# Kernel tuning notes

Hardware: AMD Instinct MI355X
Metric: run time of the kernel (lower is better)

Reference implementation:

```python
import jax, jax.numpy as jnp
import numpy as np

# --- static mask-construction config (mirrors FlexAttnFunc.init_mask args) ---
B = 1
L_F, L_H, L_W = 8, 20, 36      # latent_shape[2:]
A_F, A_H, A_W = 8, 1, 1        # action_shape[2:]
PATCH = (1, 2, 2)
CHUNK = 1
PAD = 176
WINDOW = 6
DIM, HEADS, DHEAD = 1536, 12, 128
EPS = 1e-5


def _make_ids():
    lf, lh, lw = L_F // PATCH[0], L_H // PATCH[1], L_W // PATCH[2]
    lat_seq = np.repeat(np.arange(B), lf * lh * lw)
    act_seq = np.repeat(np.arange(B), A_F * A_H * A_W)
    seq = np.concatenate([lat_seq, lat_seq, act_seq, act_seq])
    lat_fr = np.broadcast_to(np.arange(L_F)[None, :, None, None], (B, L_F, lh, lw)).reshape(-1)
    act_fr = np.broadcast_to(np.arange(A_F)[None, :, None, None], (B, A_F, A_H, A_W)).reshape(-1)
    fr = np.concatenate([lat_fr // CHUNK * 2] * 2 + [act_fr // CHUNK * 2 + 1] * 2)
    nz = np.concatenate([np.zeros_like(lat_fr), np.ones_like(lat_fr),
                         np.zeros_like(act_fr), np.ones_like(act_fr)])
    pad = np.full(PAD, -1, dtype=np.int64)
    return (np.concatenate([seq, pad]).astype(np.int32),
            np.concatenate([fr, pad]).astype(np.int32),
            np.concatenate([nz, pad]).astype(np.int32))


def setup_inputs() -> dict:
    key = jax.random.key(0)
    ks = jax.random.split(key, 8)
    seq, fr, nz = _make_ids()
    S = seq.shape[0]  # 3072
    sd = 0.02
    return {
        'x': jax.random.normal(ks[0], (1, S, DIM), jnp.float32),
        'Wq': jax.random.normal(ks[1], (DIM, DIM), jnp.float32) * sd,
        'bq': jnp.zeros((DIM,), jnp.float32),
        'Wk': jax.random.normal(ks[2], (DIM, DIM), jnp.float32) * sd,
        'bk': jnp.zeros((DIM,), jnp.float32),
        'Wv': jax.random.normal(ks[3], (DIM, DIM), jnp.float32) * sd,
        'bv': jnp.zeros((DIM,), jnp.float32),
        'gq': 1.0 + jax.random.normal(ks[4], (DIM,), jnp.float32) * sd,
        'gk': 1.0 + jax.random.normal(ks[5], (DIM,), jnp.float32) * sd,
        'Wo': jax.random.normal(ks[6], (DIM, DIM), jnp.float32) * sd,
        'bo': jnp.zeros((DIM,), jnp.float32),
        'seq_ids': jnp.asarray(seq),
        'frame_ids': jnp.asarray(fr),
        'noise_ids': jnp.asarray(nz),
        'window_size': WINDOW,
    }


def _rms(u, g):
    # torch.nn.RMSNorm over last dim (size heads*dim_head), elementwise affine
    return u * jax.lax.rsqrt(jnp.mean(u * u, axis=-1, keepdims=True) + EPS) * g


def _mask(seq_ids, frame_ids, noise_ids, window_size):
    sq, sk = seq_ids[:, None], seq_ids[None, :]
    fq, fk = frame_ids[:, None], frame_ids[None, :]
    nq, nk = noise_ids[:, None], noise_ids[None, :]
    seq_ok = (sq == sk) & (sq >= 0) & (sk >= 0)
    c2c = (nq == 1) & (nk == 1) & (fk <= fq)      # clean->clean, block causal incl self
    n2c = (nq == 0) & (nk == 1) & (fk < fq)       # noise->clean, causal excl self
    n2n = (nq == 0) & (nk == 0) & (fk == fq)      # noise->noise, same frame only
    win = jnp.abs(fq - fk) <= window_size
    return (c2c | n2c | n2n) & seq_ok & win


def reference(x, Wq, bq, Wk, bk, Wv, bv, gq, gk, Wo, bo,
              seq_ids, frame_ids, noise_ids, window_size):
    S = x.shape[1]
    q = _rms(x @ Wq + bq, gq)[0].reshape(S, HEADS, DHEAD)
    k = _rms(x @ Wk + bk, gk)[0].reshape(S, HEADS, DHEAD)
    v = (x @ Wv + bv)[0].reshape(S, HEADS, DHEAD)
    mask = _mask(seq_ids, frame_ids, noise_ids, window_size)  # [S,S] bool
    scores = jnp.einsum('qhd,khd->hqk', q, k) * (DHEAD ** -0.5)
    scores = jnp.where(mask[None], scores, jnp.float32(-1e9))
    attn = jax.nn.softmax(scores, axis=-1)
    o = jnp.einsum('hqk,khd->qhd', attn, v)
    # zero out padded (fully-masked) query rows
    o = o * (seq_ids >= 0).astype(o.dtype)[:, None, None]
    y = o.reshape(1, S, HEADS * DHEAD) @ Wo + bo
    return y
```

## Files before the change

kernel.cpp:

```cpp
#include <hip/hip_runtime.h>
#include <hip/hip_bf16.h>
#include <stdint.h>

typedef __bf16 bf16x8 __attribute__((ext_vector_type(8)));
typedef float f32x4 __attribute__((ext_vector_type(4)));

__device__ __forceinline__ unsigned short f2bf(float f) {
  union { float f; unsigned int u; } v; v.f = f;
  unsigned int u = v.u;
  unsigned int r = (u + 0x7fffu + ((u >> 16) & 1u)) >> 16;
  return (unsigned short)r;
}
__device__ __forceinline__ float bf2f(unsigned short s) {
  union { unsigned int u; float f; } v; v.u = ((unsigned int)s) << 16; return v.f;
}

__global__ __launch_bounds__(256) void setup(
    const float* __restrict__ x,
    const float* __restrict__ Wq, const float* __restrict__ Wk,
    const float* __restrict__ Wv, const float* __restrict__ Wo,
    const int* __restrict__ seq, const int* __restrict__ fr,
    const int* __restrict__ nz, const int* __restrict__ wsz,
    unsigned short* __restrict__ x_bf, unsigned short* __restrict__ wt,
    unsigned long long* __restrict__ tbm, unsigned char* __restrict__ mb,
    float* __restrict__ ssq, int S) {
  __shared__ __align__(16) unsigned char smu[16384];
  int b = blockIdx.x, tid = threadIdx.x;
  if (b < 1152) {
    int base = b * 1024 + tid;
    for (int j = 0; j < 4; j++) {
      int i = base + j * 256;
      float4 v = ((const float4*)x)[i];
      ushort4 o;
      o.x = f2bf(v.x); o.y = f2bf(v.y); o.z = f2bf(v.z); o.w = f2bf(v.w);
      ((ushort4*)x_bf)[i] = o;
    }
  } else if (b < 3456) {
    int id = b - 1152;
    int z = id / 576, rem = id % 576;
    int kx = rem % 24, ny = rem / 24;
    const float* W = z == 0 ? Wq : (z == 1 ? Wk : (z == 2 ? Wv : Wo));
    unsigned short (*t)[65] = (unsigned short(*)[65])smu;
    int k0 = kx * 64, n0 = ny * 64;
    const int N = 1536, K = 1536;
    for (int i = 0; i < 16; i++) {
      int e = tid + i * 256;
      int r = e >> 6, c = e & 63;
      t[r][c] = f2bf(W[(size_t)(k0 + r) * N + n0 + c]);
    }
    __syncthreads();
    for (int i = 0; i < 16; i++) {
      int e = tid + i * 256;
      int r = e >> 6, c = e & 63;
      wt[(size_t)(z * 1536 + n0 + r) * K + k0 + c] = t[c][r];
    }
  } else if (b == 3456) {
    int* ks_ = (int*)smu;
    unsigned int* tm_ = (unsigned int*)(smu + 12288);
    int W = wsz[0];
    for (int i = tid; i < S; i += 256) {
      int sq = seq[i];
      ks_[i] = (sq < 0) ? 0 : ((1 << 9) | ((nz[i] & 1) << 8) | (fr[i] & 15) | (sq << 10));
    }
    for (int i = tid; i < 6144; i += 256) ssq[i] = 0.f;
    __syncthreads();
    for (int t = tid; t < S / 32; t += 256) {
      unsigned int m = 0;
      for (int j = 0; j < 32; j++) {
        int a = ks_[t * 32 + j];
        if (a & (1 << 9)) m |= (a & (1 << 8)) ? (1u << (16 + (a & 15))) : (1u << (a & 15));
      }
      tm_[t] = m;
    }
    __syncthreads();
    for (int qg = tid; qg < S / 16; qg += 256) {
      unsigned int allowed = 0;
      for (int j = 0; j < 16; j++) {
        int a = ks_[qg * 16 + j];
        if (!(a & (1 << 9))) continue;
        int fq = a & 15, nq = (a >> 8) & 1;
        int lo = fq - W; if (lo < 0) lo = 0;
        unsigned int lom = ~((1u << lo) - 1);
        if (nq) allowed |= (((1u << (fq + 1)) - 1) & lom) << 16;
        else    allowed |= ((((1u << fq) - 1) & lom) << 16) | (1u << fq);
      }
      unsigned long long b0 = 0, b1 = 0;
      for (int t = 0; t < 96; t++)
        if (tm_[t] & allowed) { if (t < 64) b0 |= 1ull << t; else b1 |= 1ull << (t - 64); }
      tbm[qg * 2] = b0; tbm[qg * 2 + 1] = b1;
    }
  } else {
    int qg = b - 3457;
    int* ks_ = (int*)smu;
    int W = wsz[0];
    for (int i = tid; i < S; i += 256) {
      int sq = seq[i];
      ks_[i] = (sq < 0) ? 0 : ((1 << 9) | ((nz[i] & 1) << 8) | (fr[i] & 15) | (sq << 10));
    }
    __syncthreads();
    int wave = tid >> 6, lane = tid & 63, quad = lane >> 4, l16 = lane & 15;
    int aq[4];
    for (int r = 0; r < 4; r++) aq[r] = ks_[qg * 16 + quad * 4 + r];
    for (int t = wave; t < 96; t += 4) {
      int ak[2] = { ks_[t * 32 + l16], ks_[t * 32 + 16 + l16] };
      unsigned int byte = 0;
      for (int nt = 0; nt < 2; nt++) {
        int a = ak[nt];
        int kfr = a & 15, knz = (a >> 8) & 1, kvb = (a >> 9) & 1, ksq = a >> 10;
        for (int r = 0; r < 4; r++) {
          int bq_ = aq[r];
          int qfr = bq_ & 15, qnz = (bq_ >> 8) & 1, qvb = (bq_ >> 9) & 1, qsq = bq_ >> 10;
          bool ok  = qvb && kvb && (qsq == ksq);
          bool c2c = qnz && knz && (kfr <= qfr);
          bool n2c = !qnz && knz && (kfr < qfr);
          bool n2n = !qnz && !knz && (kfr == qfr);
          int df = qfr - kfr; df = df < 0 ? -df : df;
          if ((c2c || n2c || n2n) && ok && (df <= W)) byte |= 1u << (nt * 4 + r);
        }
      }
      mb[((size_t)qg * 96 + t) * 64 + lane] = (unsigned char)byte;
    }
  }
}

__global__ __launch_bounds__(512) void gemm_qkv(
    const unsigned short* __restrict__ A, const unsigned short* __restrict__ Bt,
    const float* __restrict__ bq, const float* __restrict__ bk, const float* __restrict__ bv,
    const float* __restrict__ gq, const float* __restrict__ gk,
    unsigned short* __restrict__ qt, unsigned short* __restrict__ ktb,
    unsigned short* __restrict__ vtb, float* __restrict__ ssq, int S) {
  __shared__ __align__(16) unsigned short smem[65536];
  int tid = threadIdx.x, wid = tid >> 6, lane = tid & 63;
  int quad = lane >> 4, l16 = lane & 15;
  int m0 = blockIdx.x * 256, n0 = blockIdx.y * 256;
  int wm = (wid >> 2) * 128;
  int wn = (wid & 3) * 64;
  int lr = lane >> 3;
  int lsw = ((lane & 7) ^ lr) * 8;
  int sx = l16 & 7;

  f32x4 acc[8][4] = {};

#define STAGEQ(t_, q_) do { \
    if ((t_) < 24) { \
      int b_ = (t_) & 1; \
      int k0_ = (t_) * 64; \
      unsigned short* ldsb = ((q_) < 2) ? (smem + b_ * 16384) : (smem + 32768 + b_ * 16384); \
      const unsigned short* gsrc = ((q_) < 2) ? A : Bt; \
      int rbase = ((q_) < 2) ? m0 : n0; \
      int lo8_ = ((q_) & 1) * 8; \
      for (int c_ = 0; c_ < 2; c_++) { \
        int chunk = lo8_ + c_ * 16 + wid; \
        const unsigned short* src = gsrc + (size_t)(rbase + chunk * 8 + lr) * 1536 + k0_ + lsw; \
        __builtin_amdgcn_global_load_lds( \
            (const __attribute__((address_space(1))) unsigned int*)src, \
            (__attribute__((address_space(3))) unsigned int*)(ldsb + chunk * 512 + lane * 8), 16, 0, 0); \
      } \
    } } while (0)

  STAGEQ(0, 0); STAGEQ(0, 1); STAGEQ(0, 2); STAGEQ(0, 3);
  STAGEQ(1, 0);
  asm volatile("s_waitcnt vmcnt(2)" ::: "memory");
  __builtin_amdgcn_s_barrier();
  __builtin_amdgcn_sched_barrier(0);

#define PHASE(p) do { \
    constexpr int q_ = (p) & 3; \
    constexpr int tb_ = (p) >> 2; \
    constexpr int k8_ = (q_ >> 1) * 4; \
    constexpr int mi0_ = (q_ & 1) * 4; \
    unsigned short* Ab = smem + tb_ * 16384; \
    unsigned short* Bb = smem + 32768 + tb_ * 16384; \
    int so_ = ((k8_ + quad) ^ sx) << 3; \
    if constexpr ((q_ & 1) == 0) { \
      for (int nj = 0; nj < 4; nj++) \
        bfr[nj] = *(const bf16x8*)&Bb[(wn + nj * 16 + l16) * 64 + so_]; \
    } \
    bf16x8 af[4]; \
    for (int ii = 0; ii < 4; ii++) \
      af[ii] = *(const bf16x8*)&Ab[(wm + (mi0_ + ii) * 16 + l16) * 64 + so_]; \
    STAGEQ(2 * i + kStT[p], kStQ[p]); \
    __builtin_amdgcn_sched_barrier(0); \
    __builtin_amdgcn_s_barrier(); \
    asm volatile("s_waitcnt lgkmcnt(0)" ::: "memory"); \
    __builtin_amdgcn_sched_barrier(0); \
    __builtin_amdgcn_s_setprio(1); \
    for (int ii = 0; ii < 4; ii++) \
      for (int nj = 0; nj < 4; nj++) \
        acc[mi0_ + ii][nj] = __builtin_amdgcn_mfma_f32_16x16x32_bf16(af[ii], bfr[nj], acc[mi0_ + ii][nj], 0, 0, 0); \
    __builtin_amdgcn_s_setprio(0); \
    if constexpr (q_ == 3) { asm volatile("s_waitcnt vmcnt(2)" ::: "memory"); } \
    __builtin_amdgcn_s_barrier(); \
    __builtin_amdgcn_sched_barrier(0); \
  } while (0)

  constexpr int kStT[8] = {1, 1, 1, 2, 2, 2, 2, 3};
  constexpr int kStQ[8] = {1, 2, 3, 0, 1, 2, 3, 0};

  for (int i = 0; i < 12; i++) {
    bf16x8 bfr[4];
    PHASE(0); PHASE(1); PHASE(2); PHASE(3);
    PHASE(4); PHASE(5); PHASE(6); PHASE(7);
  }
#undef PHASE
#undef STAGEQ

  int region = (n0 >= 3072) ? 2 : (n0 >= 1536 ? 1 : 0);
  int cbase = n0 - region * 1536;
  int hh0 = cbase >> 7;
  unsigned short* Cs = smem;
  if (region < 2) {
    const float* bias = region == 0 ? bq : bk;
    float* ssqp = ssq + region * 3072;
    float ss[8][4] = {};
    for (int nj = 0; nj < 4; nj++) {
      int col = wn + nj * 16 + l16;
      float b = bias[cbase + col];
      float G = (region == 1) ? gq[cbase + col] * gk[cbase + col] : 1.0f;
      for (int mi = 0; mi < 8; mi++)
        for (int r = 0; r < 4; r++) {
          float v = acc[mi][nj][r] + b;
          ss[mi][r] += v * v;
          Cs[(wm + mi * 16 + quad * 4 + r) * 256 + col] = f2bf(v * G);
        }
    }
    for (int mi = 0; mi < 8; mi++)
      for (int r = 0; r < 4; r++) {
        float v = ss[mi][r];
        for (int o = 1; o < 16; o <<= 1) v += __shfl_xor(v, o);
        if (l16 == 0)
          atomicAdd(&ssqp[m0 + wm + mi * 16 + quad * 4 + r], v);
      }
    __syncthreads();
    unsigned short* outb = (region == 0 ? qt : ktb);
    for (int p = 0; p < 16; p++) {
      int o = p * 4096 + tid * 8;
      int row = o >> 8, col = o & 255;
      size_t dst = (size_t)(hh0 + (col >> 7)) * 393216 + (size_t)(m0 + row) * 128 + (col & 127);
      *(uint4*)&outb[dst] = *(const uint4*)&Cs[o];
    }
  } else {
    for (int nj = 0; nj < 4; nj++) {
      int col = wn + nj * 16 + l16;
      float b = bv[cbase + col];
      int c8 = l16 * 8;
      for (int mi = 0; mi < 8; mi++)
        for (int r = 0; r < 4; r++) {
          int sp = wm + mi * 16 + quad * 4 + r;
          Cs[col * 256 + (sp ^ c8)] = f2bf(acc[mi][nj][r] + b);
        }
    }
    __syncthreads();
    for (int hh = 0; hh < 2; hh++) {
      unsigned short* outp = vtb + ((size_t)(hh0 + hh) * 96 + (m0 >> 5)) * 4096;
      for (int p = 0; p < 8; p++) {
        int o = p * 4096 + tid * 8;
        int tile = o >> 12, rem = o & 4095;
        int dd = rem >> 5, s31 = rem & 31;
        int laddr = (hh * 128 + dd) * 256 + ((tile * 32 + s31) ^ ((dd & 15) * 8));
        *(uint4*)&outp[o] = *(const uint4*)&Cs[laddr];
      }
    }
  }
}

__global__ __launch_bounds__(256) void gemm_wo(
    const unsigned short* __restrict__ A, const unsigned short* __restrict__ Bt,
    const float* __restrict__ bias, float* __restrict__ C, int M, int N, int K) {
  __shared__ __align__(16) unsigned short As[128 * 64];
  __shared__ __align__(16) unsigned short Bs[64 * 64];
  int tid = threadIdx.x, wave = tid >> 6, lane = tid & 63;
  int quad = lane >> 4, l16 = lane & 15;
  int m0 = blockIdx.x * 128, n0 = blockIdx.y * 64;
  int wm = (wave & 1) * 64, wn = (wave >> 1) * 32;
  int lr = lane >> 3;
  int lc = ((lane & 7) ^ lr) * 8;
  int sx = l16 & 7;
  f32x4 acc[4][2] = {};
  for (int k0 = 0; k0 < K; k0 += 64) {
    for (int c = 0; c < 4; c++) {
      int chunk = wave * 4 + c;
      int row = chunk * 8 + lr;
      const unsigned short* ga = &A[(size_t)(m0 + row) * K + k0 + lc];
      __builtin_amdgcn_global_load_lds(
          (const __attribute__((address_space(1))) unsigned int*)ga,
          (__attribute__((address_space(3))) unsigned int*)(As + chunk * 512), 16, 0, 0);
    }
    for (int c = 0; c < 2; c++) {
      int chunk = wave * 2 + c;
      int row = chunk * 8 + lr;
      const unsigned short* gb = &Bt[(size_t)(n0 + row) * K + k0 + lc];
      __builtin_amdgcn_global_load_lds(
          (const __attribute__((address_space(1))) unsigned int*)gb,
          (__attribute__((address_space(3))) unsigned int*)(Bs + chunk * 512), 16, 0, 0);
    }
    __syncthreads();
    for (int kk = 0; kk < 64; kk += 32) {
      int k8 = kk >> 3;
      int sw = ((k8 + quad) ^ sx) << 3;
      bf16x8 af[4], bfr[2];
      for (int i = 0; i < 4; i++)
        af[i] = *(const bf16x8*)&As[(wm + i * 16 + l16) * 64 + sw];
      for (int j = 0; j < 2; j++)
        bfr[j] = *(const bf16x8*)&Bs[(wn + j * 16 + l16) * 64 + sw];
      for (int i = 0; i < 4; i++)
        for (int j = 0; j < 2; j++)
          acc[i][j] = __builtin_amdgcn_mfma_f32_16x16x32_bf16(af[i], bfr[j], acc[i][j], 0, 0, 0);
    }
    __syncthreads();
  }
  for (int j = 0; j < 2; j++) {
    int col = n0 + wn + j * 16 + l16;
    float b = bias[col];
    for (int i = 0; i < 4; i++)
      for (int r = 0; r < 4; r++)
        C[(size_t)(m0 + wm + i * 16 + quad * 4 + r) * N + col] = acc[i][j][r] + b;
  }
}

__global__ __launch_bounds__(256) void attn(
    const unsigned short* __restrict__ qt,
    const unsigned short* __restrict__ kt,
    const unsigned short* __restrict__ vt,
    const unsigned char* __restrict__ mb,
    const unsigned long long* __restrict__ tbm,
    const float* __restrict__ ssq,
    unsigned short* __restrict__ op0b, unsigned short* __restrict__ op1b,
    float* __restrict__ lp, int S) {
  const int h = blockIdx.x;
  const int qb64 = blockIdx.y;
  const int split = blockIdx.z;
  int tid = threadIdx.x, wave = tid >> 6, lane = tid & 63;
  int quad = lane >> 4, l16 = lane & 15;
  const float scale = 0.088388347648318447f;

  __shared__ __align__(16) unsigned short Ks[2][4096];
  __shared__ __align__(16) unsigned short Vs[2][4096];
  __shared__ __align__(16) unsigned short pshare[4][16][40];

  int qg = qb64 * 4 + wave;
  unsigned long long bm0 = tbm[(qb64 * 4) * 2]     | tbm[(qb64 * 4 + 1) * 2] |
                           tbm[(qb64 * 4 + 2) * 2] | tbm[(qb64 * 4 + 3) * 2];
  unsigned long long bm1 = tbm[(qb64 * 4) * 2 + 1]     | tbm[(qb64 * 4 + 1) * 2 + 1] |
                           tbm[(qb64 * 4 + 2) * 2 + 1] | tbm[(qb64 * 4 + 3) * 2 + 1];
  unsigned long long wb0 = tbm[qg * 2], wb1 = tbm[qg * 2 + 1];

  const unsigned short* kth = kt + (size_t)h * 96 * 4096;
  const unsigned short* vth = vt + (size_t)h * 96 * 4096;
  const unsigned char* mbq = mb + (size_t)qg * 96 * 64;

  bf16x8 qf[4];
  {
    const unsigned short* qp = qt + ((size_t)(h * 192 + qg) * 16 + l16) * 128 + quad * 8;
    for (int ks = 0; ks < 4; ks++) qf[ks] = *(const bf16x8*)&qp[ks * 32];
  }
  float qs[4];
  for (int r = 0; r < 4; r++) {
    int row = qb64 * 64 + wave * 16 + quad * 4 + r;
    qs[r] = rsqrtf(ssq[row] * (1.0f / 1536.0f) + 1e-5f) * scale;
  }
  const float* ssk = ssq + 3072;

  f32x4 oacc[8] = {};
  f32x4 lacc = {};
  const __bf16 onebf = (__bf16)1.0f;
  const bf16x8 ones = {onebf, onebf, onebf, onebf, onebf, onebf, onebf, onebf};

#define POP(dst) do { \
    if (bm0) { dst = __builtin_ctzll(bm0); bm0 &= bm0 - 1; } \
    else if (bm1) { dst = 64 + __builtin_ctzll(bm1); bm1 &= bm1 - 1; } \
    else dst = -1; } while (0)

#define STAGE(t_, b_) do { \
    for (int j = 0; j < 2; j++) { \
      int slot = j * 256 + tid; \
      int key = slot >> 4, cc = slot & 15; \
      const unsigned short* src = kth + (size_t)(t_) * 4096 + key * 128 + (cc ^ (key & 15)) * 8; \
      __builtin_amdgcn_global_load_lds( \
          (const __attribute__((address_space(1))) unsigned int*)src, \
          (__attribute__((address_space(3))) unsigned int*)(&Ks[b_][0] + j * 2048 + wave * 512), \
          16, 0, 0); \
    } \
    for (int j = 0; j < 2; j++) { \
      int slot = j * 256 + tid; \
      int row = slot >> 2, cc = slot & 3; \
      const unsigned short* src = vth + (size_t)(t_) * 4096 + row * 32 + (cc ^ ((row >> 1) & 3)) * 8; \
      __builtin_amdgcn_global_load_lds( \
          (const __attribute__((address_space(1))) unsigned int*)src, \
          (__attribute__((address_space(3))) unsigned int*)(&Vs[b_][0] + j * 2048 + wave * 512), \
          16, 0, 0); \
    } } while (0)

  int t, dsc;
  if (split) POP(dsc);
  POP(t);
  unsigned int mbyte = 0;
  float kss0 = 0.f, kss1 = 0.f;
  if (t >= 0) {
    STAGE(t, 0);
    mbyte = mbq[t * 64 + lane];
    kss0 = ssk[t * 32 + l16]; kss1 = ssk[t * 32 + 16 + l16];
  }
  asm volatile("s_waitcnt vmcnt(0)" ::: "memory");
  __builtin_amdgcn_s_barrier();
  int buf = 0;

  while (t >= 0) {
    POP(dsc);
    int tn; POP(tn);
    unsigned int mbyte2 = 0;
    float nss0 = 0.f, nss1 = 0.f;
    if (tn >= 0) {
      STAGE(tn, buf ^ 1);
      mbyte2 = mbq[tn * 64 + lane];
      nss0 = ssk[tn * 32 + l16]; nss1 = ssk[tn * 32 + 16 + l16];
      asm volatile("s_waitcnt vmcnt(7)" ::: "memory");
    } else {
      asm volatile("s_waitcnt vmcnt(0)" ::: "memory");
    }
    __builtin_amdgcn_s_barrier();
    __builtin_amdgcn_sched_barrier(0);

    bool live = (t < 64) ? ((wb0 >> t) & 1) : ((wb1 >> (t - 64)) & 1);
    if (live) {
      f32x4 sacc[2] = {};
      __builtin_amdgcn_s_setprio(1);
      for (int nt = 0; nt < 2; nt++) {
        int key = nt * 16 + l16;
        for (int ks = 0; ks < 4; ks++) {
          int cc = (ks * 4 + quad) ^ l16;
          bf16x8 kf = *(const bf16x8*)&Ks[buf][(key * 16 + cc) * 8];
          sacc[nt] = __builtin_amdgcn_mfma_f32_16x16x32_bf16(qf[ks], kf, sacc[nt], 0, 0, 0);
        }
      }
      __builtin_amdgcn_s_setprio(0);
      float ksc[2];
      ksc[0] = rsqrtf(kss0 * (1.0f / 1536.0f) + 1e-5f);
      ksc[1] = rsqrtf(kss1 * (1.0f / 1536.0f) + 1e-5f);
      for (int nt = 0; nt < 2; nt++)
        for (int r = 0; r < 4; r++) {
          float e = __expf(sacc[nt][r] * (qs[r] * ksc[nt]) - 16.0f);
          float p = ((mbyte >> (nt * 4 + r)) & 1) ? e : 0.0f;
          pshare[wave][quad * 4 + r][nt * 16 + l16] = f2bf(p);
        }
      __asm__ __volatile__("s_waitcnt lgkmcnt(0)" ::: "memory");
      bf16x8 pf = *(const bf16x8*)&pshare[wave][l16][quad * 8];
      __builtin_amdgcn_s_setprio(1);
      for (int d = 0; d < 8; d++) {
        int row = d * 16 + l16;
        int cc = quad ^ ((l16 >> 1) & 3);
        bf16x8 vf = *(const bf16x8*)&Vs[buf][(row * 4 + cc) * 8];
        oacc[d] = __builtin_amdgcn_mfma_f32_16x16x32_bf16(pf, vf, oacc[d], 0, 0, 0);
      }
      lacc = __builtin_amdgcn_mfma_f32_16x16x32_bf16(pf, ones, lacc, 0, 0, 0);
      __builtin_amdgcn_s_setprio(0);
    }
    __builtin_amdgcn_s_barrier();
    buf ^= 1;
    t = tn;
    mbyte = mbyte2;
    kss0 = nss0; kss1 = nss1;
  }
#undef POP
#undef STAGE

  unsigned short* po = split ? op1b : op0b;
  for (int r = 0; r < 4; r++) {
    int q = qb64 * 64 + wave * 16 + quad * 4 + r;
    float inv = (lacc[r] > 0.f) ? 1.0f / lacc[r] : 0.0f;
    for (int d = 0; d < 8; d++)
      po[((size_t)h * S + q) * 128 + d * 16 + l16] = f2bf(oacc[d][r] * inv);
    if (l16 == 0)
      lp[((size_t)split * 12 + h) * S + q] = lacc[r];
  }
}

__global__ __launch_bounds__(256) void combine(const unsigned short* __restrict__ op0b,
                                               const unsigned short* __restrict__ op1b,
                                               const float* __restrict__ lp,
                                               const int* __restrict__ seq,
                                               unsigned short* __restrict__ ob, int S) {
  int e4 = blockIdx.x * 256 + threadIdx.x;
  int idx = e4 * 4;
  int per_h = S * 128;
  int h = idx / per_h;
  int rem = idx - h * per_h;
  int q = rem >> 7, dd = rem & 127;
  float l0 = lp[(size_t)h * S + q], l1 = lp[(size_t)(12 + h) * S + q];
  float tot = l0 + l1;
  float ok = (seq[q] >= 0 && tot > 0.f) ? 1.0f / tot : 0.0f;
  float w0 = l0 * ok, w1 = l1 * ok;
  ushort4 a = ((const ushort4*)op0b)[e4];
  ushort4 b = ((const ushort4*)op1b)[e4];
  ushort4 o;
  o.x = f2bf(bf2f(a.x) * w0 + bf2f(b.x) * w1);
  o.y = f2bf(bf2f(a.y) * w0 + bf2f(b.y) * w1);
  o.z = f2bf(bf2f(a.z) * w0 + bf2f(b.z) * w1);
  o.w = f2bf(bf2f(a.w) * w0 + bf2f(b.w) * w1);
  *(ushort4*)&ob[(size_t)q * 1536 + h * 128 + dd] = o;
}

extern "C" void kernel_launch(void* const* d_in, const int* in_sizes, int n_in,
                              void* d_out, int out_size, void* d_ws, size_t ws_size,
                              hipStream_t stream) {
  const float* x  = (const float*)d_in[0];
  const float* Wq = (const float*)d_in[1];
  const float* bq = (const float*)d_in[2];
  const float* Wk = (const float*)d_in[3];
  const float* bk = (const float*)d_in[4];
  const float* Wv = (const float*)d_in[5];
  const float* bv = (const float*)d_in[6];
  const float* gq = (const float*)d_in[7];
  const float* gk = (const float*)d_in[8];
  const float* Wo = (const float*)d_in[9];
  const float* bo = (const float*)d_in[10];
  const int* seq  = (const int*)d_in[11];
  const int* fr   = (const int*)d_in[12];
  const int* nz   = (const int*)d_in[13];
  const int* wsz  = (const int*)d_in[14];
  float* out = (float*)d_out;
  const int S = in_sizes[11];
  const int D = 1536;

  char* ws = (char*)d_ws;
  size_t off = 0;
  unsigned short* x_bf = (unsigned short*)(ws + off); off += (size_t)S * D * 2;
  unsigned short* wt   = (unsigned short*)(ws + off); off += (size_t)4 * D * D * 2;
  unsigned short* qt   = (unsigned short*)(ws + off); off += (size_t)S * D * 2;
  unsigned short* ktb  = (unsigned short*)(ws + off); off += (size_t)S * D * 2;
  unsigned short* vtb  = (unsigned short*)(ws + off); off += (size_t)S * D * 2;
  unsigned short* o_bf = (unsigned short*)(ws + off); off += (size_t)S * D * 2;
  unsigned short* op0b = (unsigned short*)(ws + off); off += (size_t)S * D * 2;
  unsigned short* op1b = (unsigned short*)(ws + off); off += (size_t)S * D * 2;
  unsigned long long* tbm = (unsigned long long*)(ws + off); off += (size_t)(S / 16) * 16;
  unsigned char*  mbuf = (unsigned char*)(ws + off);  off += (size_t)(S / 16) * 96 * 64;
  float*          lp   = (float*)(ws + off);          off += (size_t)2 * 12 * S * 4;
  float*          ssq  = (float*)(ws + off);          off += (size_t)2 * 3072 * 4;

  dim3 blk(256);
  setup<<<dim3(3649), blk, 0, stream>>>(x, Wq, Wk, Wv, Wo, seq, fr, nz, wsz,
                                        x_bf, wt, tbm, mbuf, ssq, S);
  gemm_qkv<<<dim3(S / 256, 3 * D / 256), dim3(512), 0, stream>>>(x_bf, wt, bq, bk, bv, gq, gk,
                                                                 qt, ktb, vtb, ssq, S);
  attn<<<dim3(D / 128, S / 64, 2), blk, 0, stream>>>(qt, ktb, vtb, mbuf, tbm, ssq,
                                                     op0b, op1b, lp, S);
  combine<<<dim3(12 * S * 128 / 4 / 256), blk, 0, stream>>>(op0b, op1b, lp, seq, o_bf, S);
  gemm_wo<<<dim3(S / 128, D / 64), blk, 0, stream>>>(o_bf, wt + (size_t)3 * D * D,
                                                     bo, out, S, D, D);
}
```

Baseline: 271.8 us.

## Triple-buffer attention K/V, schedule heavy query blocks first, widen Wo GEMM tile

The attention loop moves from double to triple buffering of K/V tiles in LDS. This drops the trailing barrier per iteration and issues the next-next tile's loads before computing the current one. A setup block now sorts the 48 query-64 blocks by live key-tile count, and attention blocks read their query-block index from this schedule so the heaviest blocks launch first and load balances better. Separately, the output GEMM tile grows from 128x64 to 128x128 to raise reuse per block, which halves the grid and adds accumulator registers and LDS.

```diff
diff --git a/kernel.cpp b/kernel.cpp
--- a/kernel.cpp
+++ b/kernel.cpp
@@ -23,7 +23,7 @@
     const int* __restrict__ nz, const int* __restrict__ wsz,
     unsigned short* __restrict__ x_bf, unsigned short* __restrict__ wt,
     unsigned long long* __restrict__ tbm, unsigned char* __restrict__ mb,
-    float* __restrict__ ssq, int S) {
+    float* __restrict__ ssq, int* __restrict__ sched, int S) {
   __shared__ __align__(16) unsigned char smu[16384];
   int b = blockIdx.x, tid = threadIdx.x;
   if (b < 1152) {
@@ -88,6 +88,25 @@
       for (int t = 0; t < 96; t++)
         if (tm_[t] & allowed) { if (t < 64) b0 |= 1ull << t; else b1 |= 1ull << (t - 64); }
       tbm[qg * 2] = b0; tbm[qg * 2 + 1] = b1;
+    }
+    __syncthreads();
+    if (tid == 0) {
+      int cnt[48], idx[48];
+      for (int j = 0; j < 48; j++) {
+        unsigned long long u0 = tbm[(j * 4) * 2]     | tbm[(j * 4 + 1) * 2] |
+                                tbm[(j * 4 + 2) * 2] | tbm[(j * 4 + 3) * 2];
+        unsigned long long u1 = tbm[(j * 4) * 2 + 1]     | tbm[(j * 4 + 1) * 2 + 1] |
+                                tbm[(j * 4 + 2) * 2 + 1] | tbm[(j * 4 + 3) * 2 + 1];
+        cnt[j] = __popcll(u0) + __popcll(u1);
+        idx[j] = j;
+      }
+      for (int a = 0; a < 47; a++) {
+        int best = a;
+        for (int c = a + 1; c < 48; c++)
+          if (cnt[idx[c]] > cnt[idx[best]]) best = c;
+        int tmp = idx[a]; idx[a] = idx[best]; idx[best] = tmp;
+      }
+      for (int a = 0; a < 48; a++) sched[a] = idx[a];
     }
   } else {
     int qg = b - 3457;
@@ -267,29 +286,26 @@
 __global__ __launch_bounds__(256) void gemm_wo(
     const unsigned short* __restrict__ A, const unsigned short* __restrict__ Bt,
     const float* __restrict__ bias, float* __restrict__ C, int M, int N, int K) {
-  __shared__ __align__(16) unsigned short As[128 * 64];
-  __shared__ __align__(16) unsigned short Bs[64 * 64];
+  __shared__ __align__(16) unsigned short smem[16384];
+  unsigned short* As = smem;
+  unsigned short* Bs = smem + 8192;
   int tid = threadIdx.x, wave = tid >> 6, lane = tid & 63;
   int quad = lane >> 4, l16 = lane & 15;
-  int m0 = blockIdx.x * 128, n0 = blockIdx.y * 64;
-  int wm = (wave & 1) * 64, wn = (wave >> 1) * 32;
+  int m0 = blockIdx.x * 128, n0 = blockIdx.y * 128;
+  int wm = (wave & 1) * 64, wn = (wave >> 1) * 64;
   int lr = lane >> 3;
   int lc = ((lane & 7) ^ lr) * 8;
   int sx = l16 & 7;
-  f32x4 acc[4][2] = {};
+  f32x4 acc[4][4] = {};
   for (int k0 = 0; k0 < K; k0 += 64) {
     for (int c = 0; c < 4; c++) {
       int chunk = wave * 4 + c;
       int row = chunk * 8 + lr;
       const unsigned short* ga = &A[(size_t)(m0 + row) * K + k0 + lc];
+      const unsigned short* gb = &Bt[(size_t)(n0 + row) * K + k0 + lc];
       __builtin_amdgcn_global_load_lds(
           (const __attribute__((address_space(1))) unsigned int*)ga,
           (__attribute__((address_space(3))) unsigned int*)(As + chunk * 512), 16, 0, 0);
-    }
-    for (int c = 0; c < 2; c++) {
-      int chunk = wave * 2 + c;
-      int row = chunk * 8 + lr;
-      const unsigned short* gb = &Bt[(size_t)(n0 + row) * K + k0 + lc];
       __builtin_amdgcn_global_load_lds(
           (const __attribute__((address_space(1))) unsigned int*)gb,
           (__attribute__((address_space(3))) unsigned int*)(Bs + chunk * 512), 16, 0, 0);
@@ -298,18 +314,18 @@
     for (int kk = 0; kk < 64; kk += 32) {
       int k8 = kk >> 3;
       int sw = ((k8 + quad) ^ sx) << 3;
-      bf16x8 af[4], bfr[2];
+      bf16x8 af[4], bfr[4];
       for (int i = 0; i < 4; i++)
         af[i] = *(const bf16x8*)&As[(wm + i * 16 + l16) * 64 + sw];
-      for (int j = 0; j < 2; j++)
+      for (int j = 0; j < 4; j++)
         bfr[j] = *(const bf16x8*)&Bs[(wn + j * 16 + l16) * 64 + sw];
       for (int i = 0; i < 4; i++)
-        for (int j = 0; j < 2; j++)
+        for (int j = 0; j < 4; j++)
           acc[i][j] = __builtin_amdgcn_mfma_f32_16x16x32_bf16(af[i], bfr[j], acc[i][j], 0, 0, 0);
     }
     __syncthreads();
   }
-  for (int j = 0; j < 2; j++) {
+  for (int j = 0; j < 4; j++) {
     int col = n0 + wn + j * 16 + l16;
     float b = bias[col];
     for (int i = 0; i < 4; i++)
@@ -325,17 +341,18 @@
     const unsigned char* __restrict__ mb,
     const unsigned long long* __restrict__ tbm,
     const float* __restrict__ ssq,
+    const int* __restrict__ sched,
     unsigned short* __restrict__ op0b, unsigned short* __restrict__ op1b,
     float* __restrict__ lp, int S) {
   const int h = blockIdx.x;
-  const int qb64 = blockIdx.y;
+  const int qb64 = sched[blockIdx.y];
   const int split = blockIdx.z;
   int tid = threadIdx.x, wave = tid >> 6, lane = tid & 63;
   int quad = lane >> 4, l16 = lane & 15;
   const float scale = 0.088388347648318447f;
 
-  __shared__ __align__(16) unsigned short Ks[2][4096];
-  __shared__ __align__(16) unsigned short Vs[2][4096];
+  __shared__ __align__(16) unsigned short KsF[3 * 4096];
+  __shared__ __align__(16) unsigned short VsF[3 * 4096];
   __shared__ __align__(16) unsigned short pshare[4][16][40];
 
   int qg = qb64 * 4 + wave;
@@ -378,7 +395,7 @@
       const unsigned short* src = kth + (size_t)(t_) * 4096 + key * 128 + (cc ^ (key & 15)) * 8; \
       __builtin_amdgcn_global_load_lds( \
           (const __attribute__((address_space(1))) unsigned int*)src, \
-          (__attribute__((address_space(3))) unsigned int*)(&Ks[b_][0] + j * 2048 + wave * 512), \
+          (__attribute__((address_space(3))) unsigned int*)(&KsF[(b_) * 4096] + j * 2048 + wave * 512), \
           16, 0, 0); \
     } \
     for (int j = 0; j < 2; j++) { \
@@ -387,60 +404,65 @@
       const unsigned short* src = vth + (size_t)(t_) * 4096 + row * 32 + (cc ^ ((row >> 1) & 3)) * 8; \
       __builtin_amdgcn_global_load_lds( \
           (const __attribute__((address_space(1))) unsigned int*)src, \
-          (__attribute__((address_space(3))) unsigned int*)(&Vs[b_][0] + j * 2048 + wave * 512), \
+          (__attribute__((address_space(3))) unsigned int*)(&VsF[(b_) * 4096] + j * 2048 + wave * 512), \
           16, 0, 0); \
     } } while (0)
 
-  int t, dsc;
+  int tA, tB, dsc;
   if (split) POP(dsc);
-  POP(t);
-  unsigned int mbyte = 0;
-  float kss0 = 0.f, kss1 = 0.f;
-  if (t >= 0) {
-    STAGE(t, 0);
-    mbyte = mbq[t * 64 + lane];
-    kss0 = ssk[t * 32 + l16]; kss1 = ssk[t * 32 + 16 + l16];
-  }
-  asm volatile("s_waitcnt vmcnt(0)" ::: "memory");
-  __builtin_amdgcn_s_barrier();
-  int buf = 0;
-
-  while (t >= 0) {
-    POP(dsc);
-    int tn; POP(tn);
-    unsigned int mbyte2 = 0;
-    float nss0 = 0.f, nss1 = 0.f;
-    if (tn >= 0) {
-      STAGE(tn, buf ^ 1);
-      mbyte2 = mbq[tn * 64 + lane];
-      nss0 = ssk[tn * 32 + l16]; nss1 = ssk[tn * 32 + 16 + l16];
-      asm volatile("s_waitcnt vmcnt(7)" ::: "memory");
-    } else {
-      asm volatile("s_waitcnt vmcnt(0)" ::: "memory");
-    }
+  POP(tA);
+  unsigned int mbA = 0, mbB = 0;
+  float aS0 = 0.f, aS1 = 0.f, bS0 = 0.f, bS1 = 0.f;
+  if (tA >= 0) {
+    STAGE(tA, 0);
+    mbA = mbq[tA * 64 + lane];
+    aS0 = ssk[tA * 32 + l16]; aS1 = ssk[tA * 32 + 16 + l16];
+  }
+  POP(dsc); POP(tB);
+  if (tB >= 0) {
+    STAGE(tB, 1);
+    mbB = mbq[tB * 64 + lane];
+    bS0 = ssk[tB * 32 + l16]; bS1 = ssk[tB * 32 + 16 + l16];
+  }
+  int bufA = 0, bufB = 1, bufC = 2;
+
+  while (tA >= 0) {
+    if (tB >= 0) { asm volatile("s_waitcnt vmcnt(7)" ::: "memory"); }
+    else         { asm volatile("s_waitcnt vmcnt(0)" ::: "memory"); }
     __builtin_amdgcn_s_barrier();
     __builtin_amdgcn_sched_barrier(0);
 
-    bool live = (t < 64) ? ((wb0 >> t) & 1) : ((wb1 >> (t - 64)) & 1);
+    int tC; POP(dsc); POP(tC);
+    unsigned int mbC = 0; float cS0 = 0.f, cS1 = 0.f;
+    if (tC >= 0) {
+      STAGE(tC, bufC);
+      mbC = mbq[tC * 64 + lane];
+      cS0 = ssk[tC * 32 + l16]; cS1 = ssk[tC * 32 + 16 + l16];
+    }
+    __builtin_amdgcn_sched_barrier(0);
+
+    bool live = (tA < 64) ? ((wb0 >> tA) & 1) : ((wb1 >> (tA - 64)) & 1);
     if (live) {
+      const unsigned short* Kb = &KsF[bufA * 4096];
+      const unsigned short* Vb = &VsF[bufA * 4096];
       f32x4 sacc[2] = {};
       __builtin_amdgcn_s_setprio(1);
       for (int nt = 0; nt < 2; nt++) {
         int key = nt * 16 + l16;
         for (int ks = 0; ks < 4; ks++) {
           int cc = (ks * 4 + quad) ^ l16;
-          bf16x8 kf = *(const bf16x8*)&Ks[buf][(key * 16 + cc) * 8];
+          bf16x8 kf = *(const bf16x8*)&Kb[(key * 16 + cc) * 8];
           sacc[nt] = __builtin_amdgcn_mfma_f32_16x16x32_bf16(qf[ks], kf, sacc[nt], 0, 0, 0);
         }
       }
       __builtin_amdgcn_s_setprio(0);
       float ksc[2];
-      ksc[0] = rsqrtf(kss0 * (1.0f / 1536.0f) + 1e-5f);
-      ksc[1] = rsqrtf(kss1 * (1.0f / 1536.0f) + 1e-5f);
+      ksc[0] = rsqrtf(aS0 * (1.0f / 1536.0f) + 1e-5f);
+      ksc[1] = rsqrtf(aS1 * (1.0f / 1536.0f) + 1e-5f);
       for (int nt = 0; nt < 2; nt++)
         for (int r = 0; r < 4; r++) {
           float e = __expf(sacc[nt][r] * (qs[r] * ksc[nt]) - 16.0f);
-          float p = ((mbyte >> (nt * 4 + r)) & 1) ? e : 0.0f;
+          float p = ((mbA >> (nt * 4 + r)) & 1) ? e : 0.0f;
           pshare[wave][quad * 4 + r][nt * 16 + l16] = f2bf(p);
         }
       __asm__ __volatile__("s_waitcnt lgkmcnt(0)" ::: "memory");
@@ -449,17 +471,16 @@
       for (int d = 0; d < 8; d++) {
         int row = d * 16 + l16;
         int cc = quad ^ ((l16 >> 1) & 3);
-        bf16x8 vf = *(const bf16x8*)&Vs[buf][(row * 4 + cc) * 8];
+        bf16x8 vf = *(const bf16x8*)&Vb[(row * 4 + cc) * 8];
         oacc[d] = __builtin_amdgcn_mfma_f32_16x16x32_bf16(pf, vf, oacc[d], 0, 0, 0);
       }
       lacc = __builtin_amdgcn_mfma_f32_16x16x32_bf16(pf, ones, lacc, 0, 0, 0);
       __builtin_amdgcn_s_setprio(0);
     }
-    __builtin_amdgcn_s_barrier();
-    buf ^= 1;
-    t = tn;
-    mbyte = mbyte2;
-    kss0 = nss0; kss1 = nss1;
+    tA = tB; tB = tC;
+    mbA = mbB; mbB = mbC;
+    aS0 = bS0; aS1 = bS1; bS0 = cS0; bS1 = cS1;
+    int tmpb = bufA; bufA = bufB; bufB = bufC; bufC = tmpb;
   }
 #undef POP
 #undef STAGE
@@ -536,15 +557,16 @@
   unsigned char*  mbuf = (unsigned char*)(ws + off);  off += (size_t)(S / 16) * 96 * 64;
   float*          lp   = (float*)(ws + off);          off += (size_t)2 * 12 * S * 4;
   float*          ssq  = (float*)(ws + off);          off += (size_t)2 * 3072 * 4;
+  int*            schd = (int*)(ws + off);            off += 64 * 4;
 
   dim3 blk(256);
   setup<<<dim3(3649), blk, 0, stream>>>(x, Wq, Wk, Wv, Wo, seq, fr, nz, wsz,
-                                        x_bf, wt, tbm, mbuf, ssq, S);
+                                        x_bf, wt, tbm, mbuf, ssq, schd, S);
   gemm_qkv<<<dim3(S / 256, 3 * D / 256), dim3(512), 0, stream>>>(x_bf, wt, bq, bk, bv, gq, gk,
                                                                  qt, ktb, vtb, ssq, S);
-  attn<<<dim3(D / 128, S / 64, 2), blk, 0, stream>>>(qt, ktb, vtb, mbuf, tbm, ssq,
+  attn<<<dim3(D / 128, S / 64, 2), blk, 0, stream>>>(qt, ktb, vtb, mbuf, tbm, ssq, schd,
                                                      op0b, op1b, lp, S);
   combine<<<dim3(12 * S * 128 / 4 / 256), blk, 0, stream>>>(op0b, op1b, lp, seq, o_bf, S);
-  gemm_wo<<<dim3(S / 128, D / 64), blk, 0, stream>>>(o_bf, wt + (size_t)3 * D * D,
-                                                     bo, out, S, D, D);
-}
+  gemm_wo<<<dim3(S / 128, D / 128), blk, 0, stream>>>(o_bf, wt + (size_t)3 * D * D,
+                                                      bo, out, S, D, D);
+}
```

Result: slower. 433.0 us (+59.3%).
